# Kernel tuning notes

Hardware: AMD Instinct MI355X
Metric: run time of the kernel (lower is better)

Reference implementation:

```python
import jax, jax.numpy as jnp
import numpy as np

B, N, OBS, HID, H = 8, 1024, 64, 192, 3
D = HID // H  # head_dim = 64
ALPHA = 0.2   # LeakyReLU negative slope
NEG = -9e15   # mask value from torch code (-9000000000000000.0)


def gat_layer(h, adj, W, a):
    """Multi-head GAT layer, math-identical to the torch per-head loop.
    h: (B,N,F_in), adj: (N,N), W: (H,F_in,D), a: (H,2D).
    Concat-score a^T [Wh_i || Wh_j] is split into a_l^T Wh_i + a_r^T Wh_j
    (broadcast-add) to avoid materializing the N^2 x 2D tensor.
    """
    Wh = jnp.einsum('bni,hid->bhnd', h, W)           # (B,H,N,D)
    d = Wh.shape[-1]
    s_i = jnp.einsum('bhnd,hd->bhn', Wh, a[:, :d])   # a_l . Wh_i
    s_j = jnp.einsum('bhnd,hd->bhn', Wh, a[:, d:])   # a_r . Wh_j
    e = s_i[..., :, None] + s_j[..., None, :]        # (B,H,N,N)
    e = jnp.where(e > 0, e, ALPHA * e)               # LeakyReLU
    e = jnp.where(adj > 0, e, NEG)                   # adjacency mask
    attn = jax.nn.softmax(e, axis=-1)                # (dropout=0 in eval)
    out = jnp.einsum('bhnm,bhmd->bhnd', attn, Wh)    # weighted aggregate
    b, nh, n, _ = out.shape
    return out.transpose(0, 2, 1, 3).reshape(b, n, nh * d)  # concat heads


def setup_inputs() -> dict:
    key = jax.random.key(0)
    k1, k2, k3, k4, k5 = jax.random.split(key, 5)
    h = jax.random.normal(k1, (B, N, OBS), dtype=jnp.float32)
    adj = jnp.ones((N, N), dtype=jnp.float32)  # graph_type='full'
    # xavier_uniform-style scale (gain=1.414)
    def xav(k, shape, fan_in, fan_out):
        lim = 1.414 * np.sqrt(6.0 / (fan_in + fan_out))
        return jax.random.uniform(k, shape, jnp.float32, -lim, lim)
    W1 = xav(k2, (H, OBS, D), OBS, D)
    a1 = xav(k3, (H, 2 * D), 2 * D, 1)
    W2 = xav(k4, (H, HID, D), HID, D)
    a2 = xav(k5, (H, 2 * D), 2 * D, 1)
    return {"h": h, "adj": adj, "W1": W1, "a1": a1, "W2": W2, "a2": a2}


def reference(h, adj, W1, a1, W2, a2):
    x = gat_layer(h, adj, W1, a1)   # (B,N,HID)
    x = jax.nn.elu(x)               # inter-layer nonlinearity
    x = gat_layer(x, adj, W2, a2)   # (B,N,HID)
    return x
```

## Files before the change

### kernel.cpp

```cpp
#include <hip/hip_runtime.h>
#include <math.h>

#define Bc   8
#define Nc   1024
#define OBSc 64
#define HIDc 192
#define NHc  3
#define Dc   64
#define ALPHAc 0.2f

typedef __attribute__((ext_vector_type(8))) _Float16 half8;
typedef __attribute__((ext_vector_type(4))) float floatx4;

__device__ __forceinline__ unsigned int enc_f32(float f) {
    unsigned int u = __float_as_uint(f);
    return (u & 0x80000000u) ? ~u : (u | 0x80000000u);
}
__device__ __forceinline__ float dec_f32(unsigned int e) {
    return __uint_as_float((e & 0x80000000u) ? (e & 0x7FFFFFFFu) : ~e);
}


__global__ __launch_bounds__(256) void proj1_kernel(
    const float* __restrict__ xin,
    const float* __restrict__ W1,
    const float* __restrict__ a,
    _Float16* __restrict__ WhT,
    float* __restrict__ si, float* __restrict__ sj,
    unsigned int* __restrict__ Menc,
    const float* __restrict__ adj,
    unsigned long long* __restrict__ adjb,
    const float* __restrict__ W2,
    _Float16* __restrict__ W2T)
{
    const int tid = threadIdx.x;
    const int bh  = blockIdx.y;

    if (bh == Bc * NHc) {
        const int px = blockIdx.x, wv = tid >> 6, lane = tid & 63;
        for (int r8 = 0; r8 < 8; ++r8) {
            const int i = px * 32 + wv * 8 + r8;
            unsigned long long word = 0;
            for (int g = 0; g < 16; ++g) {
                bool c = adj[(size_t)i * Nc + g * 64 + lane] > 0.f;
                unsigned long long bal = __ballot(c);
                if (lane == g) word = bal;
            }
            if (lane < 16) adjb[(size_t)i * 16 + lane] = word;
        }
        if (px < 12) {
            for (int e = px * 3072 + tid; e < px * 3072 + 3072; e += 256) {
                int t = e & 7, ln = (e >> 3) & 63, p = (e >> 9) & 1, nh = (e >> 10) & 1;
                int g = e >> 11; int ks = g % 6, hh = g / 6;
                int k = ks * 32 + (ln >> 4) * 8 + t;
                int d = nh * 32 + p * 16 + (ln & 15);
                W2T[e] = (_Float16)W2[((size_t)hh * HIDc + k) * Dc + d];
            }
        }
        return;
    }

    __shared__ union {
        _Float16 Bs[64][OBSc + 8];
        _Float16 Ts[64][40];
    } u;
    __shared__ float spsA_i[32], spsA_j[32], spsB_i[32], spsB_j[32];

    const int b = bh / NHc, hh = bh % NHc;
    const int row0 = blockIdx.x * 32;

    for (int e = tid; e < OBSc * 64; e += 256) {
        int k = e >> 6, d = e & 63;
        u.Bs[d][k] = (_Float16)W1[(size_t)hh * OBSc * 64 + e];
    }
    __syncthreads();

    const int lane = tid & 63, wv = tid >> 6;
    const int mblk = (wv & 1) * 16, nhalf = (wv >> 1) * 32;
    const int fr = lane & 15, fq = lane >> 4;
    floatx4 acc0 = {0.f,0.f,0.f,0.f}, acc1 = {0.f,0.f,0.f,0.f};
    const int row = row0 + mblk + fr;

#pragma unroll
    for (int ks = 0; ks < OBSc / 32; ++ks) {
        const int k0 = ks * 32 + fq * 8;
        const float* xr = xin + ((size_t)b * Nc + row) * OBSc + k0;
        float4 u0 = *(const float4*)xr;
        float4 u1 = *(const float4*)(xr + 4);
        half8 af;
        af[0] = (_Float16)u0.x; af[1] = (_Float16)u0.y;
        af[2] = (_Float16)u0.z; af[3] = (_Float16)u0.w;
        af[4] = (_Float16)u1.x; af[5] = (_Float16)u1.y;
        af[6] = (_Float16)u1.z; af[7] = (_Float16)u1.w;
        half8 b0 = *(const half8*)&u.Bs[nhalf + fr][k0];
        half8 b1 = *(const half8*)&u.Bs[nhalf + 16 + fr][k0];
        acc0 = __builtin_amdgcn_mfma_f32_16x16x32_f16(af, b0, acc0, 0, 0, 0);
        acc1 = __builtin_amdgcn_mfma_f32_16x16x32_f16(af, b1, acc1, 0, 0, 0);
    }

    const float al0 = a[hh * 2 * Dc + nhalf + fr];
    const float al1 = a[hh * 2 * Dc + nhalf + 16 + fr];
    const float ar0 = a[hh * 2 * Dc + Dc + nhalf + fr];
    const float ar1 = a[hh * 2 * Dc + Dc + nhalf + 16 + fr];
    float pi[4], pj[4];
#pragma unroll
    for (int r = 0; r < 4; ++r) {
        pi[r] = acc0[r] * al0 + acc1[r] * al1;
        pj[r] = acc0[r] * ar0 + acc1[r] * ar1;
        for (int off = 8; off >= 1; off >>= 1) {
            pi[r] += __shfl_xor(pi[r], off, 64);
            pj[r] += __shfl_xor(pj[r], off, 64);
        }
    }
    if (fr == 0) {
#pragma unroll
        for (int r = 0; r < 4; ++r) {
            int lr = mblk + fq * 4 + r;
            if (nhalf == 0) { spsA_i[lr] = pi[r]; spsA_j[lr] = pj[r]; }
            else            { spsB_i[lr] = pi[r]; spsB_j[lr] = pj[r]; }
        }
    }
    __syncthreads();
    if (tid < 64) {
        float vj = -INFINITY;
        if (tid < 32) {
            size_t g = (size_t)bh * Nc + row0 + tid;
            si[g] = spsA_i[tid] + spsB_i[tid];
            vj    = spsA_j[tid] + spsB_j[tid];
            sj[g] = vj;
        }
        float mv = vj;
        for (int off = 32; off >= 1; off >>= 1) mv = fmaxf(mv, __shfl_xor(mv, off, 64));
        if (tid == 0) atomicMax(&Menc[bh], enc_f32(mv));
    }

#pragma unroll
    for (int nt = 0; nt < 2; ++nt) {
        const int d = nhalf + nt * 16 + fr;
        floatx4 acc = nt ? acc1 : acc0;
#pragma unroll
        for (int p = 0; p < 2; ++p) {
            union { unsigned int w; _Float16 h[2]; } pk;
            pk.h[0] = (_Float16)acc[2 * p];
            pk.h[1] = (_Float16)acc[2 * p + 1];
            *(unsigned int*)&u.Ts[d][mblk + fq * 4 + 2 * p] = pk.w;
        }
    }
    __syncthreads();
    {
        const int c2 = tid >> 6, lane2 = tid & 63;
        const int fr2 = lane2 & 15, fq2 = lane2 >> 4;
        const int jt = row0 >> 5;
        uint4 v = *(const uint4*)&u.Ts[c2 * 16 + fr2][fq2 * 8];
        *(uint4*)&WhT[(size_t)(bh * 32 + jt) * 2048 + tid * 8] = v;
    }
}

__global__ __launch_bounds__(256) void proj2_kernel(
    const _Float16* __restrict__ xh,
    const _Float16* __restrict__ W2T,
    const float* __restrict__ a,
    _Float16* __restrict__ WhT,
    float* __restrict__ si, float* __restrict__ sj,
    unsigned int* __restrict__ Menc)
{
    __shared__ _Float16 Ts[64][40];
    __shared__ float spsA_i[32], spsA_j[32], spsB_i[32], spsB_j[32];

    const int tid = threadIdx.x, bh = blockIdx.y;
    const int b = bh / NHc, hh = bh % NHc;
    const int row0 = blockIdx.x * 32;
    const int lane = tid & 63, wv = tid >> 6;
    const int mblk = (wv & 1) * 16, nhalf = (wv >> 1) * 32;
    const int fr = lane & 15, fq = lane >> 4;
    const int nh = nhalf >> 5;

    floatx4 acc0 = {0.f,0.f,0.f,0.f}, acc1 = {0.f,0.f,0.f,0.f};
    const int row = row0 + mblk + fr;

#pragma unroll
    for (int ks = 0; ks < HIDc / 32; ++ks) {
        half8 af = *(const half8*)&xh[((size_t)b * Nc + row) * HIDc + ks * 32 + fq * 8];
        const _Float16* wb = W2T + (size_t)((hh * 6 + ks) * 2 + nh) * 1024 + lane * 8;
        half8 b0 = *(const half8*)wb;
        half8 b1 = *(const half8*)(wb + 512);
        acc0 = __builtin_amdgcn_mfma_f32_16x16x32_f16(af, b0, acc0, 0, 0, 0);
        acc1 = __builtin_amdgcn_mfma_f32_16x16x32_f16(af, b1, acc1, 0, 0, 0);
    }

    const float al0 = a[hh * 2 * Dc + nhalf + fr];
    const float al1 = a[hh * 2 * Dc + nhalf + 16 + fr];
    const float ar0 = a[hh * 2 * Dc + Dc + nhalf + fr];
    const float ar1 = a[hh * 2 * Dc + Dc + nhalf + 16 + fr];
    float pi[4], pj[4];
#pragma unroll
    for (int r = 0; r < 4; ++r) {
        pi[r] = acc0[r] * al0 + acc1[r] * al1;
        pj[r] = acc0[r] * ar0 + acc1[r] * ar1;
        for (int off = 8; off >= 1; off >>= 1) {
            pi[r] += __shfl_xor(pi[r], off, 64);
            pj[r] += __shfl_xor(pj[r], off, 64);
        }
    }
    if (fr == 0) {
#pragma unroll
        for (int r = 0; r < 4; ++r) {
            int lr = mblk + fq * 4 + r;
            if (nhalf == 0) { spsA_i[lr] = pi[r]; spsA_j[lr] = pj[r]; }
            else            { spsB_i[lr] = pi[r]; spsB_j[lr] = pj[r]; }
        }
    }
    __syncthreads();
    if (tid < 64) {
        float vj = -INFINITY;
        if (tid < 32) {
            size_t g = (size_t)bh * Nc + row0 + tid;
            si[g] = spsA_i[tid] + spsB_i[tid];
            vj    = spsA_j[tid] + spsB_j[tid];
            sj[g] = vj;
        }
        float mv = vj;
        for (int off = 32; off >= 1; off >>= 1) mv = fmaxf(mv, __shfl_xor(mv, off, 64));
        if (tid == 0) atomicMax(&Menc[bh], enc_f32(mv));
    }

#pragma unroll
    for (int nt = 0; nt < 2; ++nt) {
        const int d = nhalf + nt * 16 + fr;
        floatx4 acc = nt ? acc1 : acc0;
#pragma unroll
        for (int p = 0; p < 2; ++p) {
            union { unsigned int w; _Float16 h[2]; } pk;
            pk.h[0] = (_Float16)acc[2 * p];
            pk.h[1] = (_Float16)acc[2 * p + 1];
            *(unsigned int*)&Ts[d][mblk + fq * 4 + 2 * p] = pk.w;
        }
    }
    __syncthreads();
    {
        const int c2 = tid >> 6, lane2 = tid & 63;
        const int fr2 = lane2 & 15, fq2 = lane2 >> 4;
        const int jt = row0 >> 5;
        uint4 v = *(const uint4*)&Ts[c2 * 16 + fr2][fq2 * 8];
        *(uint4*)&WhT[(size_t)(bh * 32 + jt) * 2048 + tid * 8] = v;
    }
}

template <bool DO_ELU, typename OutT>
__global__ __launch_bounds__(256, 4) void aggr_kernel(
    const _Float16* __restrict__ WhT,
    const float* __restrict__ si,
    const float* __restrict__ sj,
    const unsigned int* __restrict__ Menc,
    const unsigned long long* __restrict__ adjb,
    OutT* __restrict__ out)
{
    __shared__ float red[4][64][20];
    __shared__ float zs[4][16];

    const int tid  = threadIdx.x;
    const int wv   = tid >> 6, lane = tid & 63;
    const int bh   = blockIdx.x >> 6;
    const int row0 = (blockIdx.x & 63) << 4;
    const int b    = bh / NHc, hh = bh % NHc;
    const int fr   = lane & 15, fq = lane >> 4;
    const int row  = row0 + fr;

    const float M   = dec_f32(Menc[bh]);
    const float s_i = si[(size_t)bh * Nc + row];
    const float em  = s_i + M;
    const float m_i = fmaxf(em, ALPHAc * em);

    const float* sjr = sj + (size_t)bh * Nc + fq * 8;
    const unsigned long long* arow = adjb + (size_t)row * 16;
    const _Float16* Bp = WhT + (size_t)bh * 65536 + (size_t)wv * 8 * 2048 + lane * 8;

    floatx4 acc[4] = {{0.f,0.f,0.f,0.f},{0.f,0.f,0.f,0.f},
                      {0.f,0.f,0.f,0.f},{0.f,0.f,0.f,0.f}};
    float zacc = 0.f;

    float4 sa = *(const float4*)&sjr[wv * 256];
    float4 sb = *(const float4*)&sjr[wv * 256 + 4];
    unsigned long long w = arow[(wv * 8) >> 1];
    half8 bfr0 = *(const half8*)(Bp);
    half8 bfr1 = *(const half8*)(Bp + 512);
    half8 bfr2 = *(const half8*)(Bp + 1024);
    half8 bfr3 = *(const half8*)(Bp + 1536);

#pragma unroll
    for (int s8 = 0; s8 < 8; ++s8) {
        const int s = wv * 8 + s8;
        float4 nsa, nsb; unsigned long long nw;
        half8 nb0, nb1, nb2, nb3;
        if (s8 < 7) {
            const int jn = (s + 1) * 32 - wv * 256;
            nsa = *(const float4*)&sjr[(s + 1) * 32];
            nsb = *(const float4*)&sjr[(s + 1) * 32 + 4];
            nw  = arow[(s + 1) >> 1];
            const _Float16* bn = Bp + (size_t)(s8 + 1) * 2048;
            nb0 = *(const half8*)(bn);
            nb1 = *(const half8*)(bn + 512);
            nb2 = *(const half8*)(bn + 1024);
            nb3 = *(const half8*)(bn + 1536);
            (void)jn;
        }
        const int bb = (s & 1) * 32 + fq * 8;
        const float sv[8] = {sa.x, sa.y, sa.z, sa.w, sb.x, sb.y, sb.z, sb.w};
        float p[8];
        if (w == ~0ULL) {
#pragma unroll
            for (int t = 0; t < 8; ++t) {
                float e = s_i + sv[t];
                e = fmaxf(e, ALPHAc * e) - m_i;
                p[t] = __expf(e);
            }
        } else {
#pragma unroll
            for (int t = 0; t < 8; ++t) {
                float e = s_i + sv[t];
                e = fmaxf(e, ALPHAc * e) - m_i;
                e = ((w >> (bb + t)) & 1) ? e : -1e30f;
                p[t] = __expf(e);
            }
        }
        zacc += ((p[0] + p[1]) + (p[2] + p[3])) + ((p[4] + p[5]) + (p[6] + p[7]));
        union { half8 v; _Float16 h[8]; } A;
#pragma unroll
        for (int t = 0; t < 8; ++t) A.h[t] = (_Float16)p[t];
        acc[0] = __builtin_amdgcn_mfma_f32_16x16x32_f16(A.v, bfr0, acc[0], 0, 0, 0);
        acc[1] = __builtin_amdgcn_mfma_f32_16x16x32_f16(A.v, bfr1, acc[1], 0, 0, 0);
        acc[2] = __builtin_amdgcn_mfma_f32_16x16x32_f16(A.v, bfr2, acc[2], 0, 0, 0);
        acc[3] = __builtin_amdgcn_mfma_f32_16x16x32_f16(A.v, bfr3, acc[3], 0, 0, 0);
        if (s8 < 7) {
            sa = nsa; sb = nsb; w = nw;
            bfr0 = nb0; bfr1 = nb1; bfr2 = nb2; bfr3 = nb3;
        }
    }

    zacc += __shfl_xor(zacc, 16, 64);
    zacc += __shfl_xor(zacc, 32, 64);
    if (lane < 16) zs[wv][lane] = zacc;
#pragma unroll
    for (int c = 0; c < 4; ++c)
        *(floatx4*)&red[wv][lane][c * 4] = acc[c];
    __syncthreads();

    floatx4 af = {0.f, 0.f, 0.f, 0.f};
#pragma unroll
    for (int w2 = 0; w2 < 4; ++w2) {
        floatx4 r = *(const floatx4*)&red[w2][lane][wv * 4];
        af[0] += r[0]; af[1] += r[1]; af[2] += r[2]; af[3] += r[3];
    }
#pragma unroll
    for (int reg = 0; reg < 4; ++reg) {
        const int r = fq * 4 + reg;
        const float Z = (zs[0][r] + zs[1][r]) + (zs[2][r] + zs[3][r]);
        float v = af[reg] / Z;
        if (DO_ELU) v = v > 0.f ? v : expm1f(v);
        out[((size_t)b * Nc + row0 + r) * HIDc + hh * Dc + wv * 16 + fr] = (OutT)v;
    }
}

extern "C" void kernel_launch(void* const* d_in, const int* in_sizes, int n_in,
                              void* d_out, int out_size, void* d_ws, size_t ws_size,
                              hipStream_t stream) {
    const float* h_in = (const float*)d_in[0];
    const float* adj  = (const float*)d_in[1];
    const float* W1   = (const float*)d_in[2];
    const float* a1   = (const float*)d_in[3];
    const float* W2   = (const float*)d_in[4];
    const float* a2   = (const float*)d_in[5];
    float* out = (float*)d_out;

    float* ws = (float*)d_ws;
    const size_t nWhT_f = (size_t)Bc * NHc * Dc * Nc / 2;
    const size_t nXh_f  = (size_t)Bc * Nc * HIDc / 2;
    const size_t nAb_f  = (size_t)Nc * 16 * 2;
    const size_t nW2T_f = 36864 / 2;
    const size_t nR     = (size_t)Bc * NHc * Nc;
    _Float16* WhT = (_Float16*)ws;
    _Float16* xh  = (_Float16*)(ws + nWhT_f);
    unsigned long long* adjb = (unsigned long long*)(ws + nWhT_f + nXh_f);
    _Float16* W2T = (_Float16*)(ws + nWhT_f + nXh_f + nAb_f);
    float* si = ws + nWhT_f + nXh_f + nAb_f + nW2T_f;
    float* sj = si + nR;
    unsigned int* Menc = (unsigned int*)(sj + nR);

    (void)hipMemsetAsync(Menc, 0, 48 * sizeof(unsigned int), stream);

    dim3 projGrid1(Nc / 32, Bc * NHc + 1);
    dim3 projGrid2(Nc / 32, Bc * NHc);

    proj1_kernel<<<projGrid1, 256, 0, stream>>>(
        h_in, W1, a1, WhT, si, sj, Menc, adj, adjb, W2, W2T);
    aggr_kernel<true, _Float16><<<1536, 256, 0, stream>>>(
        WhT, si, sj, Menc, adjb, xh);

    proj2_kernel<<<projGrid2, 256, 0, stream>>>(
        xh, W2T, a2, WhT, si, sj, Menc + 24);
    aggr_kernel<false, float><<<1536, 256, 0, stream>>>(
        WhT, si, sj, Menc + 24, adjb, out);
}
```

Before: 136.0 us.

## Fuse layer-1 aggregation with layer-2 projection and replace atomic max with partials

Merges the first attention aggregation, ELU and the second-layer projection into one kernel, so the intermediate activations stay in shared memory and are not written to or read back from global memory. The global atomicMax on encoded floats and its memset are replaced by per-block partial maxima that consumers reduce themselves. This removes one launch and one round trip through global memory. In exchange the fused kernel runs only 512 blocks of 384 threads, each doing 16 k-steps instead of 8, which lowers parallelism for the aggregation phase.

New measurement: 119.2 us. -12.4%, faster.

```diff
diff --git a/kernel.cpp b/kernel.cpp
--- a/kernel.cpp
+++ b/kernel.cpp
@@ -12,26 +12,13 @@
 typedef __attribute__((ext_vector_type(8))) _Float16 half8;
 typedef __attribute__((ext_vector_type(4))) float floatx4;
 
-__device__ __forceinline__ unsigned int enc_f32(float f) {
-    unsigned int u = __float_as_uint(f);
-    return (u & 0x80000000u) ? ~u : (u | 0x80000000u);
-}
-__device__ __forceinline__ float dec_f32(unsigned int e) {
-    return __uint_as_float((e & 0x80000000u) ? (e & 0x7FFFFFFFu) : ~e);
-}
-
-
-__global__ __launch_bounds__(256) void proj1_kernel(
-    const float* __restrict__ xin,
-    const float* __restrict__ W1,
-    const float* __restrict__ a,
-    _Float16* __restrict__ WhT,
-    float* __restrict__ si, float* __restrict__ sj,
-    unsigned int* __restrict__ Menc,
-    const float* __restrict__ adj,
-    unsigned long long* __restrict__ adjb,
-    const float* __restrict__ W2,
-    _Float16* __restrict__ W2T)
+
+__global__ __launch_bounds__(256) void k_proj1(
+    const float* __restrict__ xin, const float* __restrict__ W1,
+    const float* __restrict__ a1, _Float16* __restrict__ WhT,
+    float* __restrict__ si, float* __restrict__ sj, float* __restrict__ Mp1,
+    const float* __restrict__ adj, unsigned long long* __restrict__ adjb,
+    const float* __restrict__ W2, _Float16* __restrict__ W2T)
 {
     const int tid = threadIdx.x;
     const int bh  = blockIdx.y;
@@ -64,7 +51,7 @@
         _Float16 Bs[64][OBSc + 8];
         _Float16 Ts[64][40];
     } u;
-    __shared__ float spsA_i[32], spsA_j[32], spsB_i[32], spsB_j[32];
+    __shared__ float spsAi[32], spsAj[32], spsBi[32], spsBj[32];
 
     const int b = bh / NHc, hh = bh % NHc;
     const int row0 = blockIdx.x * 32;
@@ -98,10 +85,10 @@
         acc1 = __builtin_amdgcn_mfma_f32_16x16x32_f16(af, b1, acc1, 0, 0, 0);
     }
 
-    const float al0 = a[hh * 2 * Dc + nhalf + fr];
-    const float al1 = a[hh * 2 * Dc + nhalf + 16 + fr];
-    const float ar0 = a[hh * 2 * Dc + Dc + nhalf + fr];
-    const float ar1 = a[hh * 2 * Dc + Dc + nhalf + 16 + fr];
+    const float al0 = a1[hh * 2 * Dc + nhalf + fr];
+    const float al1 = a1[hh * 2 * Dc + nhalf + 16 + fr];
+    const float ar0 = a1[hh * 2 * Dc + Dc + nhalf + fr];
+    const float ar1 = a1[hh * 2 * Dc + Dc + nhalf + 16 + fr];
     float pi[4], pj[4];
 #pragma unroll
     for (int r = 0; r < 4; ++r) {
@@ -116,8 +103,8 @@
 #pragma unroll
         for (int r = 0; r < 4; ++r) {
             int lr = mblk + fq * 4 + r;
-            if (nhalf == 0) { spsA_i[lr] = pi[r]; spsA_j[lr] = pj[r]; }
-            else            { spsB_i[lr] = pi[r]; spsB_j[lr] = pj[r]; }
+            if (nhalf == 0) { spsAi[lr] = pi[r]; spsAj[lr] = pj[r]; }
+            else            { spsBi[lr] = pi[r]; spsBj[lr] = pj[r]; }
         }
     }
     __syncthreads();
@@ -125,13 +112,13 @@
         float vj = -INFINITY;
         if (tid < 32) {
             size_t g = (size_t)bh * Nc + row0 + tid;
-            si[g] = spsA_i[tid] + spsB_i[tid];
-            vj    = spsA_j[tid] + spsB_j[tid];
+            si[g] = spsAi[tid] + spsBi[tid];
+            vj    = spsAj[tid] + spsBj[tid];
             sj[g] = vj;
         }
         float mv = vj;
         for (int off = 32; off >= 1; off >>= 1) mv = fmaxf(mv, __shfl_xor(mv, off, 64));
-        if (tid == 0) atomicMax(&Menc[bh], enc_f32(mv));
+        if (tid == 0) Mp1[bh * 32 + blockIdx.x] = mv;
     }
 
 #pragma unroll
@@ -156,104 +143,200 @@
     }
 }
 
-__global__ __launch_bounds__(256) void proj2_kernel(
-    const _Float16* __restrict__ xh,
-    const _Float16* __restrict__ W2T,
-    const float* __restrict__ a,
-    _Float16* __restrict__ WhT,
-    float* __restrict__ si, float* __restrict__ sj,
-    unsigned int* __restrict__ Menc)
+__global__ __launch_bounds__(384, 2) void k_fused(
+    const _Float16* __restrict__ WhT1,
+    const float* __restrict__ si1, const float* __restrict__ sj1,
+    const float* __restrict__ Mp1, const unsigned long long* __restrict__ adjb,
+    const _Float16* __restrict__ W2T, const float* __restrict__ a2,
+    _Float16* __restrict__ WhT2,
+    float* __restrict__ si2, float* __restrict__ sj2, float* __restrict__ Mp2)
 {
-    __shared__ _Float16 Ts[64][40];
-    __shared__ float spsA_i[32], spsA_j[32], spsB_i[32], spsB_j[32];
-
-    const int tid = threadIdx.x, bh = blockIdx.y;
-    const int b = bh / NHc, hh = bh % NHc;
-    const int row0 = blockIdx.x * 32;
-    const int lane = tid & 63, wv = tid >> 6;
-    const int mblk = (wv & 1) * 16, nhalf = (wv >> 1) * 32;
+    __shared__ union {
+        struct { float red[6][64][20]; float zs[6][16]; } ag;
+        _Float16 Ts3[3][64][24];
+    } uR;
+    __shared__ _Float16 xhs[16][208];
+    __shared__ float sp2i[6][16], sp2j[6][16];
+
+    const int tid = threadIdx.x, wv = tid >> 6, lane = tid & 63;
+    const int b = blockIdx.x >> 6, c16 = blockIdx.x & 63;
+    const int row0 = c16 * 16;
+    const int hh = wv >> 1, kh = wv & 1;
+    const int bh = b * NHc + hh;
     const int fr = lane & 15, fq = lane >> 4;
-    const int nh = nhalf >> 5;
-
-    floatx4 acc0 = {0.f,0.f,0.f,0.f}, acc1 = {0.f,0.f,0.f,0.f};
-    const int row = row0 + mblk + fr;
-
-#pragma unroll
-    for (int ks = 0; ks < HIDc / 32; ++ks) {
-        half8 af = *(const half8*)&xh[((size_t)b * Nc + row) * HIDc + ks * 32 + fq * 8];
-        const _Float16* wb = W2T + (size_t)((hh * 6 + ks) * 2 + nh) * 1024 + lane * 8;
+    const int row = row0 + fr;
+
+    float mpv = Mp1[bh * 32 + (lane & 31)];
+    for (int off = 16; off >= 1; off >>= 1) mpv = fmaxf(mpv, __shfl_xor(mpv, off, 64));
+    const float s_i = si1[(size_t)bh * Nc + row];
+    const float em  = s_i + mpv;
+    const float m_i = fmaxf(em, ALPHAc * em);
+
+    const float* sjr = sj1 + (size_t)bh * Nc;
+    const unsigned long long* arow = adjb + (size_t)row * 16;
+    const _Float16* Bp = WhT1 + (size_t)bh * 65536 + (size_t)kh * 32768 + lane * 8;
+
+    floatx4 acc[4] = {{0.f,0.f,0.f,0.f},{0.f,0.f,0.f,0.f},
+                      {0.f,0.f,0.f,0.f},{0.f,0.f,0.f,0.f}};
+    float zacc = 0.f;
+
+    float4 sa = *(const float4*)&sjr[(kh * 16) * 32 + fq * 8];
+    float4 sb = *(const float4*)&sjr[(kh * 16) * 32 + fq * 8 + 4];
+    unsigned long long w = arow[(kh * 16) >> 1];
+    half8 bfr0 = *(const half8*)(Bp);
+    half8 bfr1 = *(const half8*)(Bp + 512);
+    half8 bfr2 = *(const half8*)(Bp + 1024);
+    half8 bfr3 = *(const half8*)(Bp + 1536);
+
+#pragma unroll
+    for (int s16 = 0; s16 < 16; ++s16) {
+        const int s = kh * 16 + s16;
+        float4 nsa, nsb; unsigned long long nw;
+        half8 nb0, nb1, nb2, nb3;
+        if (s16 < 15) {
+            const int jn = (s + 1) * 32 + fq * 8;
+            nsa = *(const float4*)&sjr[jn];
+            nsb = *(const float4*)&sjr[jn + 4];
+            nw  = arow[(s + 1) >> 1];
+            const _Float16* bn = Bp + (size_t)(s16 + 1) * 2048;
+            nb0 = *(const half8*)(bn);
+            nb1 = *(const half8*)(bn + 512);
+            nb2 = *(const half8*)(bn + 1024);
+            nb3 = *(const half8*)(bn + 1536);
+        }
+        const int bb = (s & 1) * 32 + fq * 8;
+        const float sv[8] = {sa.x, sa.y, sa.z, sa.w, sb.x, sb.y, sb.z, sb.w};
+        float p[8];
+        if (w == ~0ULL) {
+#pragma unroll
+            for (int t = 0; t < 8; ++t) {
+                float e = s_i + sv[t];
+                e = fmaxf(e, ALPHAc * e) - m_i;
+                p[t] = __expf(e);
+            }
+        } else {
+#pragma unroll
+            for (int t = 0; t < 8; ++t) {
+                float e = s_i + sv[t];
+                e = fmaxf(e, ALPHAc * e) - m_i;
+                e = ((w >> (bb + t)) & 1) ? e : -1e30f;
+                p[t] = __expf(e);
+            }
+        }
+        zacc += ((p[0] + p[1]) + (p[2] + p[3])) + ((p[4] + p[5]) + (p[6] + p[7]));
+        union { half8 v; _Float16 h[8]; } A;
+#pragma unroll
+        for (int t = 0; t < 8; ++t) A.h[t] = (_Float16)p[t];
+        acc[0] = __builtin_amdgcn_mfma_f32_16x16x32_f16(A.v, bfr0, acc[0], 0, 0, 0);
+        acc[1] = __builtin_amdgcn_mfma_f32_16x16x32_f16(A.v, bfr1, acc[1], 0, 0, 0);
+        acc[2] = __builtin_amdgcn_mfma_f32_16x16x32_f16(A.v, bfr2, acc[2], 0, 0, 0);
+        acc[3] = __builtin_amdgcn_mfma_f32_16x16x32_f16(A.v, bfr3, acc[3], 0, 0, 0);
+        if (s16 < 15) {
+            sa = nsa; sb = nsb; w = nw;
+            bfr0 = nb0; bfr1 = nb1; bfr2 = nb2; bfr3 = nb3;
+        }
+    }
+
+    zacc += __shfl_xor(zacc, 16, 64);
+    zacc += __shfl_xor(zacc, 32, 64);
+    if (lane < 16) uR.ag.zs[wv][lane] = zacc;
+#pragma unroll
+    for (int c = 0; c < 4; ++c)
+        *(floatx4*)&uR.ag.red[wv][lane][c * 4] = acc[c];
+    __syncthreads();
+
+    {
+        const int w0 = hh * 2;
+#pragma unroll
+        for (int cc = 0; cc < 2; ++cc) {
+            const int c = kh * 2 + cc;
+#pragma unroll
+            for (int reg = 0; reg < 4; ++reg) {
+                const int r = fq * 4 + reg;
+                const float af = uR.ag.red[w0][lane][c * 4 + reg]
+                               + uR.ag.red[w0 + 1][lane][c * 4 + reg];
+                const float Z = uR.ag.zs[w0][r] + uR.ag.zs[w0 + 1][r];
+                float v = af / Z;
+                v = v > 0.f ? v : expm1f(v);
+                xhs[r][hh * 64 + c * 16 + fr] = (_Float16)v;
+            }
+        }
+    }
+    __syncthreads();
+
+    floatx4 a2c0 = {0.f,0.f,0.f,0.f}, a2c1 = {0.f,0.f,0.f,0.f};
+#pragma unroll
+    for (int ks = 0; ks < 6; ++ks) {
+        half8 af2 = *(const half8*)&xhs[fr][ks * 32 + fq * 8];
+        const _Float16* wb = W2T + (size_t)((hh * 6 + ks) * 2 + kh) * 1024 + lane * 8;
         half8 b0 = *(const half8*)wb;
         half8 b1 = *(const half8*)(wb + 512);
-        acc0 = __builtin_amdgcn_mfma_f32_16x16x32_f16(af, b0, acc0, 0, 0, 0);
-        acc1 = __builtin_amdgcn_mfma_f32_16x16x32_f16(af, b1, acc1, 0, 0, 0);
-    }
-
-    const float al0 = a[hh * 2 * Dc + nhalf + fr];
-    const float al1 = a[hh * 2 * Dc + nhalf + 16 + fr];
-    const float ar0 = a[hh * 2 * Dc + Dc + nhalf + fr];
-    const float ar1 = a[hh * 2 * Dc + Dc + nhalf + 16 + fr];
-    float pi[4], pj[4];
-#pragma unroll
-    for (int r = 0; r < 4; ++r) {
-        pi[r] = acc0[r] * al0 + acc1[r] * al1;
-        pj[r] = acc0[r] * ar0 + acc1[r] * ar1;
-        for (int off = 8; off >= 1; off >>= 1) {
-            pi[r] += __shfl_xor(pi[r], off, 64);
-            pj[r] += __shfl_xor(pj[r], off, 64);
-        }
-    }
-    if (fr == 0) {
-#pragma unroll
-        for (int r = 0; r < 4; ++r) {
-            int lr = mblk + fq * 4 + r;
-            if (nhalf == 0) { spsA_i[lr] = pi[r]; spsA_j[lr] = pj[r]; }
-            else            { spsB_i[lr] = pi[r]; spsB_j[lr] = pj[r]; }
-        }
-    }
-    __syncthreads();
-    if (tid < 64) {
-        float vj = -INFINITY;
-        if (tid < 32) {
-            size_t g = (size_t)bh * Nc + row0 + tid;
-            si[g] = spsA_i[tid] + spsB_i[tid];
-            vj    = spsA_j[tid] + spsB_j[tid];
-            sj[g] = vj;
-        }
+        a2c0 = __builtin_amdgcn_mfma_f32_16x16x32_f16(af2, b0, a2c0, 0, 0, 0);
+        a2c1 = __builtin_amdgcn_mfma_f32_16x16x32_f16(af2, b1, a2c1, 0, 0, 0);
+    }
+
+    {
+        const float* a2h = a2 + hh * 2 * Dc;
+        const float al0 = a2h[kh * 32 + fr];
+        const float al1 = a2h[kh * 32 + 16 + fr];
+        const float ar0 = a2h[Dc + kh * 32 + fr];
+        const float ar1 = a2h[Dc + kh * 32 + 16 + fr];
+#pragma unroll
+        for (int reg = 0; reg < 4; ++reg) {
+            float pi = a2c0[reg] * al0 + a2c1[reg] * al1;
+            float pj = a2c0[reg] * ar0 + a2c1[reg] * ar1;
+            for (int off = 8; off >= 1; off >>= 1) {
+                pi += __shfl_xor(pi, off, 64);
+                pj += __shfl_xor(pj, off, 64);
+            }
+            if (fr == 0) {
+                sp2i[wv][fq * 4 + reg] = pi;
+                sp2j[wv][fq * 4 + reg] = pj;
+            }
+        }
+    }
+    __syncthreads();
+
+    if (kh == 0 && lane < 16) {
+        const int r = lane;
+        float vi = sp2i[wv][r] + sp2i[wv + 1][r];
+        float vj = sp2j[wv][r] + sp2j[wv + 1][r];
+        si2[(size_t)bh * Nc + row0 + r] = vi;
+        sj2[(size_t)bh * Nc + row0 + r] = vj;
         float mv = vj;
-        for (int off = 32; off >= 1; off >>= 1) mv = fmaxf(mv, __shfl_xor(mv, off, 64));
-        if (tid == 0) atomicMax(&Menc[bh], enc_f32(mv));
-    }
-
-#pragma unroll
-    for (int nt = 0; nt < 2; ++nt) {
-        const int d = nhalf + nt * 16 + fr;
-        floatx4 acc = nt ? acc1 : acc0;
+        for (int off = 8; off >= 1; off >>= 1) mv = fmaxf(mv, __shfl_xor(mv, off, 64));
+        if (r == 0) Mp2[bh * 64 + c16] = mv;
+    }
+#pragma unroll
+    for (int cc = 0; cc < 2; ++cc) {
+        const int d = kh * 32 + cc * 16 + fr;
+        floatx4 av = cc ? a2c1 : a2c0;
 #pragma unroll
         for (int p = 0; p < 2; ++p) {
-            union { unsigned int w; _Float16 h[2]; } pk;
-            pk.h[0] = (_Float16)acc[2 * p];
-            pk.h[1] = (_Float16)acc[2 * p + 1];
-            *(unsigned int*)&Ts[d][mblk + fq * 4 + 2 * p] = pk.w;
-        }
-    }
-    __syncthreads();
+            union { unsigned int w2; _Float16 h[2]; } pk;
+            pk.h[0] = (_Float16)av[2 * p];
+            pk.h[1] = (_Float16)av[2 * p + 1];
+            *(unsigned int*)&uR.Ts3[hh][d][fq * 4 + 2 * p] = pk.w2;
+        }
+    }
+    __syncthreads();
+
     {
-        const int c2 = tid >> 6, lane2 = tid & 63;
-        const int fr2 = lane2 & 15, fq2 = lane2 >> 4;
-        const int jt = row0 >> 5;
-        uint4 v = *(const uint4*)&Ts[c2 * 16 + fr2][fq2 * 8];
-        *(uint4*)&WhT[(size_t)(bh * 32 + jt) * 2048 + tid * 8] = v;
+        const int hh3 = tid / 128, rem = tid % 128, d3 = rem >> 1, rr = rem & 1;
+        uint4 v = *(const uint4*)&uR.Ts3[hh3][d3][rr * 8];
+        const int bh3 = b * NHc + hh3;
+        const int jt = c16 >> 1;
+        const int c3 = d3 >> 4;
+        const int fqp = (c16 & 1) * 2 + rr;
+        *(uint4*)&WhT2[((((size_t)(bh3 * 32 + jt) * 4 + c3) * 64) + fqp * 16 + (d3 & 15)) * 8] = v;
     }
 }
 
-template <bool DO_ELU, typename OutT>
-__global__ __launch_bounds__(256, 4) void aggr_kernel(
+__global__ __launch_bounds__(256, 4) void k_aggr2(
     const _Float16* __restrict__ WhT,
-    const float* __restrict__ si,
-    const float* __restrict__ sj,
-    const unsigned int* __restrict__ Menc,
-    const unsigned long long* __restrict__ adjb,
-    OutT* __restrict__ out)
+    const float* __restrict__ si, const float* __restrict__ sj,
+    const float* __restrict__ Mp2, const unsigned long long* __restrict__ adjb,
+    float* __restrict__ out)
 {
     __shared__ float red[4][64][20];
     __shared__ float zs[4][16];
@@ -266,9 +349,11 @@
     const int fr   = lane & 15, fq = lane >> 4;
     const int row  = row0 + fr;
 
-    const float M   = dec_f32(Menc[bh]);
+    float mpv = Mp2[bh * 64 + lane];
+    for (int off = 32; off >= 1; off >>= 1) mpv = fmaxf(mpv, __shfl_xor(mpv, off, 64));
+
     const float s_i = si[(size_t)bh * Nc + row];
-    const float em  = s_i + M;
+    const float em  = s_i + mpv;
     const float m_i = fmaxf(em, ALPHAc * em);
 
     const float* sjr = sj + (size_t)bh * Nc + fq * 8;
@@ -293,7 +378,6 @@
         float4 nsa, nsb; unsigned long long nw;
         half8 nb0, nb1, nb2, nb3;
         if (s8 < 7) {
-            const int jn = (s + 1) * 32 - wv * 256;
             nsa = *(const float4*)&sjr[(s + 1) * 32];
             nsb = *(const float4*)&sjr[(s + 1) * 32 + 4];
             nw  = arow[(s + 1) >> 1];
@@ -302,7 +386,6 @@
             nb1 = *(const half8*)(bn + 512);
             nb2 = *(const half8*)(bn + 1024);
             nb3 = *(const half8*)(bn + 1536);
-            (void)jn;
         }
         const int bb = (s & 1) * 32 + fq * 8;
         const float sv[8] = {sa.x, sa.y, sa.z, sa.w, sb.x, sb.y, sb.z, sb.w};
@@ -355,9 +438,7 @@
     for (int reg = 0; reg < 4; ++reg) {
         const int r = fq * 4 + reg;
         const float Z = (zs[0][r] + zs[1][r]) + (zs[2][r] + zs[3][r]);
-        float v = af[reg] / Z;
-        if (DO_ELU) v = v > 0.f ? v : expm1f(v);
-        out[((size_t)b * Nc + row0 + r) * HIDc + hh * Dc + wv * 16 + fr] = (OutT)v;
+        out[((size_t)b * Nc + row0 + r) * HIDc + hh * Dc + wv * 16 + fr] = af[reg] / Z;
     }
 }
 
@@ -374,30 +455,25 @@
 
     float* ws = (float*)d_ws;
     const size_t nWhT_f = (size_t)Bc * NHc * Dc * Nc / 2;
-    const size_t nXh_f  = (size_t)Bc * Nc * HIDc / 2;
     const size_t nAb_f  = (size_t)Nc * 16 * 2;
     const size_t nW2T_f = 36864 / 2;
     const size_t nR     = (size_t)Bc * NHc * Nc;
-    _Float16* WhT = (_Float16*)ws;
-    _Float16* xh  = (_Float16*)(ws + nWhT_f);
-    unsigned long long* adjb = (unsigned long long*)(ws + nWhT_f + nXh_f);
-    _Float16* W2T = (_Float16*)(ws + nWhT_f + nXh_f + nAb_f);
-    float* si = ws + nWhT_f + nXh_f + nAb_f + nW2T_f;
-    float* sj = si + nR;
-    unsigned int* Menc = (unsigned int*)(sj + nR);
-
-    (void)hipMemsetAsync(Menc, 0, 48 * sizeof(unsigned int), stream);
-
-    dim3 projGrid1(Nc / 32, Bc * NHc + 1);
-    dim3 projGrid2(Nc / 32, Bc * NHc);
-
-    proj1_kernel<<<projGrid1, 256, 0, stream>>>(
-        h_in, W1, a1, WhT, si, sj, Menc, adj, adjb, W2, W2T);
-    aggr_kernel<true, _Float16><<<1536, 256, 0, stream>>>(
-        WhT, si, sj, Menc, adjb, xh);
-
-    proj2_kernel<<<projGrid2, 256, 0, stream>>>(
-        xh, W2T, a2, WhT, si, sj, Menc + 24);
-    aggr_kernel<false, float><<<1536, 256, 0, stream>>>(
-        WhT, si, sj, Menc + 24, adjb, out);
+    _Float16* WhT1 = (_Float16*)ws;
+    _Float16* WhT2 = (_Float16*)(ws + nWhT_f);
+    unsigned long long* adjb = (unsigned long long*)(ws + 2 * nWhT_f);
+    _Float16* W2T  = (_Float16*)(ws + 2 * nWhT_f + nAb_f);
+    float* si1 = ws + 2 * nWhT_f + nAb_f + nW2T_f;
+    float* sj1 = si1 + nR;
+    float* si2 = sj1 + nR;
+    float* sj2 = si2 + nR;
+    float* Mp1 = sj2 + nR;
+    float* Mp2 = Mp1 + 768;
+
+    k_proj1<<<dim3(Nc / 32, Bc * NHc + 1), 256, 0, stream>>>(
+        h_in, W1, a1, WhT1, si1, sj1, Mp1, adj, adjb, W2, W2T);
+
+    k_fused<<<512, 384, 0, stream>>>(
+        WhT1, si1, sj1, Mp1, adjb, W2T, a2, WhT2, si2, sj2, Mp2);
+
+    k_aggr2<<<1536, 256, 0, stream>>>(WhT2, si2, sj2, Mp2, adjb, out);
 }
```
